# Optimization experiments

Measured on AMD Instinct MI355X. Metric: run time of the kernel, lower is better.

## Reference

```python
import jax, jax.numpy as jnp
import numpy as np

B = 2
H_GRID, W_GRID, RADIUS = 48, 48, 3
D_MODEL, N_HEADS, D_HEAD = 512, 8, 64
N = H_GRID * W_GRID          # 2304 tokens
WSIZE = (2 * RADIUS + 1) ** 2  # 49 neighbors per token
D_ACT = D_HEAD                # d_head even -> d_act = d_head
SCALE = D_ACT ** -0.5
NEG = -1e9


def _grid_neighbors():
    rr = np.arange(N) // W_GRID
    cc = np.arange(N) % W_GRID
    off = np.arange(-RADIUS, RADIUS + 1)
    dr, dc = np.meshgrid(off, off, indexing='ij')
    dr, dc = dr.ravel(), dc.ravel()
    nr = rr[:, None] + dr[None, :]
    nc = cc[:, None] + dc[None, :]
    valid = (nr >= 0) & (nr < H_GRID) & (nc >= 0) & (nc < W_GRID)
    idx = np.clip(nr, 0, H_GRID - 1) * W_GRID + np.clip(nc, 0, W_GRID - 1)
    pos = np.stack([rr, cc], axis=-1).astype(np.float32)
    return idx.astype(np.int32), valid, pos


def setup_inputs() -> dict:
    key = jax.random.key(0)
    ks = jax.random.split(key, 8)
    idx, valid, pos = _grid_neighbors()
    s = D_MODEL ** -0.5
    return {
        'x': jax.random.normal(ks[0], (B, N, D_MODEL), jnp.float32),
        'positions': jnp.asarray(pos),
        'W_Q': jax.random.normal(ks[1], (D_MODEL, N_HEADS * D_HEAD), jnp.float32) * s,
        'W_K': jax.random.normal(ks[2], (D_MODEL, N_HEADS * D_HEAD), jnp.float32) * s,
        'W_V': jax.random.normal(ks[3], (D_MODEL, N_HEADS * D_HEAD), jnp.float32) * s,
        'W_O': jax.random.normal(ks[4], (N_HEADS * D_HEAD, D_MODEL), jnp.float32) * s,
        # learnable active-subspace basis per head (near-identity init, QR'd in fwd)
        'U': jnp.eye(D_HEAD, D_ACT)[None] + 0.05 * jax.random.normal(ks[5], (N_HEADS, D_HEAD, D_ACT), jnp.float32),
        # per-head rotation generator frequencies: theta = dr . freqs per 2x2 block
        'freqs': 0.5 * jax.random.normal(ks[6], (N_HEADS, 2, D_HEAD // 2), jnp.float32),
        'neighbor_index': jnp.asarray(idx),
        'neighbor_mask': jnp.asarray(valid),
    }


def reference(x, positions, W_Q, W_K, W_V, W_O, U, freqs, neighbor_index, neighbor_mask):
    Bt, Nt, _ = x.shape

    def heads(h):  # (B,N,H*d) -> (B,H,N,d)
        return h.reshape(Bt, Nt, N_HEADS, D_HEAD).transpose(0, 2, 1, 3)

    Q = heads(x @ W_Q)
    K = heads(x @ W_K)
    V = heads(x @ W_V)

    # Active subspace projection Pi_act = U_ortho U_ortho^T, applied as x@U@U^T
    U_ortho = jnp.linalg.qr(U)[0]                       # (H, d, d_act)
    Q = jnp.einsum('bhnd,hde,hfe->bhnf', Q, U_ortho, U_ortho)
    K = jnp.einsum('bhnd,hde,hfe->bhnf', K, U_ortho, U_ortho)

    # per-(i,j) relative rotation: block-diagonal 2x2 rotations with
    # angles theta[h,n,w,p] = (r_j - r_i) . freqs[h,:,p]
    drel = positions[neighbor_index] - positions[:, None, :]   # (N,W,2)
    theta = jnp.einsum('nwc,hcp->hnwp', drel, freqs)           # (H,N,W,d/2)
    cos, sin = jnp.cos(theta), jnp.sin(theta)

    K_loc = K[:, :, neighbor_index]                            # (B,H,N,W,d) gather
    Ke, Ko = K_loc[..., 0::2], K_loc[..., 1::2]
    Kr_e = cos[None] * Ke - sin[None] * Ko
    Kr_o = sin[None] * Ke + cos[None] * Ko
    K_rot = jnp.stack([Kr_e, Kr_o], axis=-1).reshape(K_loc.shape)

    scores = jnp.einsum('bhnd,bhnwd->bhnw', Q, K_rot) * SCALE
    scores = jnp.where(neighbor_mask[None, None], scores, NEG)
    w = jax.nn.softmax(scores, axis=-1)

    V_loc = V[:, :, neighbor_index]                            # (B,H,N,W,d)
    out = jnp.einsum('bhnw,bhnwd->bhnd', w, V_loc)
    out = out.transpose(0, 2, 1, 3).reshape(Bt, Nt, N_HEADS * D_HEAD)
    return out @ W_O
```

## Files before the change

### kernel.cpp

```cpp
#include <hip/hip_runtime.h>
#include <math.h>


#define BB 2
#define HGRID 48
#define WGRID 48
#define NNODE (HGRID*WGRID)
#define RAD 3
#define WSZ 49
#define DMODEL 512
#define NHEAD 8
#define SCALE 0.125f
#define MROWS (BB*NNODE)
#define TPAD 141

typedef _Float16 f16;
typedef __attribute__((ext_vector_type(8))) _Float16 f16x8;
typedef __attribute__((ext_vector_type(2))) _Float16 h2;
typedef __attribute__((ext_vector_type(4))) float f32x4;

typedef union { f16x8 v8; h2 h[4]; } pack8;

#if __has_builtin(__builtin_amdgcn_fdot2)
__device__ __forceinline__ float fdot2(h2 a, h2 b, float c) {
    return __builtin_amdgcn_fdot2(a, b, c, false);
}
#else
__device__ __forceinline__ float fdot2(h2 a, h2 b, float c) {
    return fmaf((float)a.x, (float)b.x, fmaf((float)a.y, (float)b.y, c));
}
#endif

__global__ void convert_all(const float* __restrict__ x,
                            const float* __restrict__ WQ, const float* __restrict__ WK,
                            const float* __restrict__ WV, const float* __restrict__ WO,
                            f16* __restrict__ x2, f16* __restrict__ Wall) {
    int id = blockIdx.x * 256 + threadIdx.x;
    if (id < MROWS * 64) {
        int r = id >> 6, c8 = (id & 63) << 3;
        float4 a = *(const float4*)&x[(size_t)r * 512 + c8];
        float4 b = *(const float4*)&x[(size_t)r * 512 + c8 + 4];
        f16 o[8] = {(f16)a.x, (f16)a.y, (f16)a.z, (f16)a.w,
                    (f16)b.x, (f16)b.y, (f16)b.z, (f16)b.w};
        *(f16x8*)&x2[(size_t)r * 512 + c8] = *(f16x8*)o;
        return;
    }
    id -= MROWS * 64;
    if (id >= 2048 * 64) return;
    int np = id >> 6;
    int kb = (id & 63) << 3;
    const float* S;
    int n;
    if (np < 1536) { int t = np >> 9; n = np & 511; S = (t == 0) ? WQ : (t == 1) ? WK : WV; }
    else           { n = np - 1536;  S = WO; }
    f16 o[8];
#pragma unroll
    for (int i = 0; i < 8; ++i) o[i] = (f16)S[(size_t)(kb + i) * 512 + n];
    *(f16x8*)&Wall[(size_t)np * 512 + kb] = *(f16x8*)o;
}

template<int MODE>
__global__ __launch_bounds__(256)
void mgemm(const f16* __restrict__ A, const f16* __restrict__ Bt,
           f16* __restrict__ Qh, f16* __restrict__ Kh, f16* __restrict__ Vh,
           float* __restrict__ Cf, const float* __restrict__ freqs) {
    __shared__ f16 As[128 * 64];
    __shared__ f16 Bs[128 * 64];

    const int tid = threadIdx.x;
    const int l = tid & 63, wid = tid >> 6;
    const int m0 = blockIdx.y * 128;
    const int n0 = blockIdx.x * 128;
    const int wm = (wid >> 1) * 64, wn = (wid & 1) * 64;
    const int fr = l & 15, fk = l >> 4;
    const int srow = l >> 3, slot = l & 7;

    f32x4 acc[4][4];
#pragma unroll
    for (int m = 0; m < 4; ++m)
#pragma unroll
        for (int n = 0; n < 4; ++n) acc[m][n] = (f32x4){0.f, 0.f, 0.f, 0.f};

    for (int kt = 0; kt < 8; ++kt) {
        const int k0 = kt * 64;
#pragma unroll
        for (int j = 0; j < 4; ++j) {
            const int r = wid * 32 + j * 8 + srow;
            const int cA = (slot ^ (r & 7)) * 8;
            const f16* gA = A + (size_t)(m0 + r) * 512 + k0 + cA;
            __builtin_amdgcn_global_load_lds(
                (const __attribute__((address_space(1))) unsigned int*)gA,
                (__attribute__((address_space(3))) unsigned int*)(As + wid * 2048 + j * 512),
                16, 0, 0);
            const f16* gB = Bt + (size_t)(n0 + r) * 512 + k0 + cA;
            __builtin_amdgcn_global_load_lds(
                (const __attribute__((address_space(1))) unsigned int*)gB,
                (__attribute__((address_space(3))) unsigned int*)(Bs + wid * 2048 + j * 512),
                16, 0, 0);
        }
        asm volatile("s_waitcnt vmcnt(0)" ::: "memory");
        __syncthreads();

        f16x8 af[4][2], bfr[4][2];
#pragma unroll
        for (int m = 0; m < 4; ++m) {
            const int row = wm + m * 16 + fr;
#pragma unroll
            for (int kk = 0; kk < 2; ++kk) {
                const int b = (kk * 64 + fk * 16) ^ ((row & 7) << 4);
                af[m][kk] = *(const f16x8*)((const char*)As + row * 128 + b);
            }
        }
#pragma unroll
        for (int n = 0; n < 4; ++n) {
            const int row = wn + n * 16 + fr;
#pragma unroll
            for (int kk = 0; kk < 2; ++kk) {
                const int b = (kk * 64 + fk * 16) ^ ((row & 7) << 4);
                bfr[n][kk] = *(const f16x8*)((const char*)Bs + row * 128 + b);
            }
        }
#pragma unroll
        for (int kk = 0; kk < 2; ++kk)
#pragma unroll
            for (int m = 0; m < 4; ++m)
#pragma unroll
                for (int n = 0; n < 4; ++n)
                    acc[m][n] = __builtin_amdgcn_mfma_f32_16x16x32_f16(
                        af[m][kk], bfr[n][kk], acc[m][n], 0, 0, 0);
        __syncthreads();
    }

    if (MODE == 0) {
#pragma unroll
        for (int nf = 0; nf < 4; ++nf) {
            const int ccol = n0 + wn + nf * 16 + fr;
            const int t = ccol >> 9;
            const int h = (ccol >> 6) & 7;
            const int d = ccol & 63;
            const int p = d >> 1;
            f16* Cp = (t == 0) ? Qh : (t == 1) ? Kh : Vh;
            const float fR = freqs[h * 64 + p];
            const float fC = freqs[h * 64 + 32 + p];
            const float sgn = (d & 1) ? 1.0f : -1.0f;
#pragma unroll
            for (int mf = 0; mf < 4; ++mf) {
#pragma unroll
                for (int i = 0; i < 4; ++i) {
                    const int grow = m0 + wm + mf * 16 + fk * 4 + i;
                    const int b_ = grow >= NNODE;
                    const int nn = grow - b_ * NNODE;
                    float val = acc[mf][nf][i];
                    float part = __shfl_xor(val, 1);
                    float outv = val;
                    if (t < 2) {
                        float th = (float)(nn / WGRID) * fR + (float)(nn % WGRID) * fC;
                        float sn, cs;
                        __sincosf(th, &sn, &cs);
                        outv = fmaf(sgn * part, sn, val * cs);
                    }
                    Cp[((size_t)((b_ * NHEAD + h) * NNODE + nn)) * 64 + d] = (f16)outv;
                }
            }
        }
    } else {
#pragma unroll
        for (int nf = 0; nf < 4; ++nf) {
            const int ccol = n0 + wn + nf * 16 + fr;
#pragma unroll
            for (int mf = 0; mf < 4; ++mf) {
#pragma unroll
                for (int i = 0; i < 4; ++i) {
                    const int grow = m0 + wm + mf * 16 + fk * 4 + i;
                    Cf[(size_t)grow * 512 + ccol] = acc[mf][nf][i];
                }
            }
        }
    }
}

__global__ __launch_bounds__(256, 5)
void attn5(const f16* __restrict__ Qh, const f16* __restrict__ Kh,
           const f16* __restrict__ Vh, f16* __restrict__ out2) {
    __shared__ h2 T[32 * TPAD];

    const int tid = threadIdx.x;
    const int wid = tid >> 6, lane = tid & 63;
    const int qs = lane >> 3, wg = lane & 7;

    const int bid = blockIdx.x;
    const int t  = bid % 72, bh = bid / 72;
    const int tr = t % 12,   tc = t / 12;
    const int r0 = tr * 4,   c0 = tc * 8;
    const int h  = bh & 7,   b_ = bh >> 3;

    const int lr0 = max(0, r0 - 3), lr1 = min(HGRID - 1, r0 + 6);
    const int lc0 = max(0, c0 - 3), lc1 = min(WGRID - 1, c0 + 10);
    const int NR = lr1 - lr0 + 1, NC = lc1 - lc0 + 1;

    const f16* Kb = Kh + (size_t)bh * NNODE * 64;
    const f16* Vb = Vh + (size_t)bh * NNODE * 64;

    const int rq = r0 + wid, cq = c0 + qs;
    const int nq = rq * WGRID + cq;
    const f16* qrow = Qh + ((size_t)bh * NNODE + nq) * 64;
    h2 q2[32];
#pragma unroll
    for (int j8 = 0; j8 < 8; ++j8) {
        pack8 v;
        v.v8 = *(const f16x8*)&qrow[j8 * 8];
#pragma unroll
        for (int k = 0; k < 4; ++k) q2[j8 * 4 + k] = v.h[k];
    }

    const int cnt = NR * NC * 8;
    for (int i = tid; i < cnt; i += 256) {
        const int row = i >> 3, p4 = i & 7;
        const int glr = row / NC, glc = row - glr * NC;
        const int n = (lr0 + glr) * WGRID + (lc0 + glc);
        pack8 v;
        v.v8 = *(const f16x8*)&Kb[(size_t)n * 64 + p4 * 8];
#pragma unroll
        for (int j = 0; j < 4; ++j) T[(p4 * 4 + j) * TPAD + row] = v.h[j];
    }
    __syncthreads();

    float sc[7], es[7];
    float mx = -1e30f;
#pragma unroll
    for (int k = 0; k < 7; ++k) {
        const int w = wg + 8 * k;
        sc[k] = -1e30f;
        if (w < WSZ) {
            const int dr = w / 7 - RAD, dc = w % 7 - RAD;
            const int nr = rq + dr, nc = cq + dc;
            const bool valid = ((unsigned)nr < (unsigned)HGRID) &&
                               ((unsigned)nc < (unsigned)WGRID);
            const int nrl = min(max(nr, lr0), lr1) - lr0;
            const int ncl = min(max(nc, lc0), lc1) - lc0;
            const int row = nrl * NC + ncl;
            float s = 0.0f;
#pragma unroll
            for (int j = 0; j < 32; ++j) s = fdot2(q2[j], T[j * TPAD + row], s);
            sc[k] = valid ? s * SCALE : -1e9f;
            mx = fmaxf(mx, sc[k]);
        }
    }
#pragma unroll
    for (int o = 1; o < 8; o <<= 1) mx = fmaxf(mx, __shfl_xor(mx, o));
    float sum = 0.0f;
#pragma unroll
    for (int k = 0; k < 7; ++k) {
        const int w = wg + 8 * k;
        es[k] = 0.0f;
        if (w < WSZ) { es[k] = __expf(sc[k] - mx); sum += es[k]; }
    }
#pragma unroll
    for (int o = 1; o < 8; o <<= 1) sum += __shfl_xor(sum, o);
    const float inv = 1.0f / sum;
    float esn[7];
#pragma unroll
    for (int k = 0; k < 7; ++k) esn[k] = es[k] * inv;

    __syncthreads();

    for (int i = tid; i < cnt; i += 256) {
        const int row = i >> 3, p4 = i & 7;
        const int glr = row / NC, glc = row - glr * NC;
        const int n = (lr0 + glr) * WGRID + (lc0 + glc);
        pack8 v;
        v.v8 = *(const f16x8*)&Vb[(size_t)n * 64 + p4 * 8];
#pragma unroll
        for (int j = 0; j < 4; ++j) T[(p4 * 4 + j) * TPAD + row] = v.h[j];
    }
    __syncthreads();

    const int dg = wg;
    float2 acc[4] = {{0, 0}, {0, 0}, {0, 0}, {0, 0}};
#pragma unroll
    for (int w = 0; w < WSZ; ++w) {
        const int dr = w / 7 - RAD, dc = w % 7 - RAD;
        const int nr = rq + dr, nc = cq + dc;
        const int nrl = min(max(nr, lr0), lr1) - lr0;
        const int ncl = min(max(nc, lc0), lc1) - lc0;
        const int row = nrl * NC + ncl;
        const float pw = __shfl(esn[w >> 3], (lane & 0x38) | (w & 7));
#pragma unroll
        for (int j = 0; j < 4; ++j) {
            h2 v2 = T[(dg * 4 + j) * TPAD + row];
            acc[j].x = fmaf(pw, (float)v2.x, acc[j].x);
            acc[j].y = fmaf(pw, (float)v2.y, acc[j].y);
        }
    }

    f16 o[8] = {(f16)acc[0].x, (f16)acc[0].y, (f16)acc[1].x, (f16)acc[1].y,
                (f16)acc[2].x, (f16)acc[2].y, (f16)acc[3].x, (f16)acc[3].y};
    const size_t rowb = (size_t)(b_ * NNODE + nq) * 512 + h * 64 + dg * 8;
    *(f16x8*)&out2[rowb] = *(f16x8*)o;
}

extern "C" void kernel_launch(void* const* d_in, const int* in_sizes, int n_in,
                              void* d_out, int out_size, void* d_ws, size_t ws_size,
                              hipStream_t stream) {
    const float* x     = (const float*)d_in[0];
    const float* WQ    = (const float*)d_in[2];
    const float* WK    = (const float*)d_in[3];
    const float* WV    = (const float*)d_in[4];
    const float* WO    = (const float*)d_in[5];
    const float* freqs = (const float*)d_in[7];

    const size_t HN = (size_t)16 * NNODE * 64;
    f16* Qh   = (f16*)d_ws;
    f16* Kh   = Qh + HN;
    f16* Vh   = Kh + HN;
    f16* x2   = Vh + HN;
    f16* Wall = x2 + (size_t)MROWS * 512;
    f16* Wo2  = Wall + (size_t)1536 * 512;

    convert_all<<<((MROWS + 2048) * 64 + 255) / 256, 256, 0, stream>>>(
        x, WQ, WK, WV, WO, x2, Wall);

    dim3 gqkv(12, 36);
    mgemm<0><<<gqkv, 256, 0, stream>>>(x2, Wall, Qh, Kh, Vh, nullptr, freqs);

    attn5<<<16 * 72, 256, 0, stream>>>(Qh, Kh, Vh, x2);

    dim3 go(4, 36);
    mgemm<1><<<go, 256, 0, stream>>>(x2, Wo2, nullptr, nullptr, nullptr,
                                     (float*)d_out, freqs);
}
```

Baseline: 64.82 us.

## Double-buffer GEMM LDS tiles and load K and V together in attention

The GEMM kernel now keeps two LDS buffers per operand and issues the global-to-LDS loads for the next k-tile before computing on the current one, so load latency overlaps with MFMA work. The attention kernel stages K and V tiles into separate shared arrays in one pass, which removes the second load phase and two barriers. In exchange, both kernels use twice the LDS, the attention launch bound drops from 5 to 4 blocks per SM, and the GEMM's occupancy may fall.

```diff
diff --git a/kernel.cpp b/kernel.cpp
--- a/kernel.cpp
+++ b/kernel.cpp
@@ -64,8 +64,8 @@
 void mgemm(const f16* __restrict__ A, const f16* __restrict__ Bt,
            f16* __restrict__ Qh, f16* __restrict__ Kh, f16* __restrict__ Vh,
            float* __restrict__ Cf, const float* __restrict__ freqs) {
-    __shared__ f16 As[128 * 64];
-    __shared__ f16 Bs[128 * 64];
+    __shared__ f16 As[2][128 * 64];
+    __shared__ f16 Bs[2][128 * 64];
 
     const int tid = threadIdx.x;
     const int l = tid & 63, wid = tid >> 6;
@@ -75,13 +75,7 @@
     const int fr = l & 15, fk = l >> 4;
     const int srow = l >> 3, slot = l & 7;
 
-    f32x4 acc[4][4];
-#pragma unroll
-    for (int m = 0; m < 4; ++m)
-#pragma unroll
-        for (int n = 0; n < 4; ++n) acc[m][n] = (f32x4){0.f, 0.f, 0.f, 0.f};
-
-    for (int kt = 0; kt < 8; ++kt) {
+    auto stage = [&](int buf, int kt) {
         const int k0 = kt * 64;
 #pragma unroll
         for (int j = 0; j < 4; ++j) {
@@ -90,16 +84,29 @@
             const f16* gA = A + (size_t)(m0 + r) * 512 + k0 + cA;
             __builtin_amdgcn_global_load_lds(
                 (const __attribute__((address_space(1))) unsigned int*)gA,
-                (__attribute__((address_space(3))) unsigned int*)(As + wid * 2048 + j * 512),
+                (__attribute__((address_space(3))) unsigned int*)(As[buf] + wid * 2048 + j * 512),
                 16, 0, 0);
             const f16* gB = Bt + (size_t)(n0 + r) * 512 + k0 + cA;
             __builtin_amdgcn_global_load_lds(
                 (const __attribute__((address_space(1))) unsigned int*)gB,
-                (__attribute__((address_space(3))) unsigned int*)(Bs + wid * 2048 + j * 512),
+                (__attribute__((address_space(3))) unsigned int*)(Bs[buf] + wid * 2048 + j * 512),
                 16, 0, 0);
         }
-        asm volatile("s_waitcnt vmcnt(0)" ::: "memory");
-        __syncthreads();
+    };
+
+    f32x4 acc[4][4];
+#pragma unroll
+    for (int m = 0; m < 4; ++m)
+#pragma unroll
+        for (int n = 0; n < 4; ++n) acc[m][n] = (f32x4){0.f, 0.f, 0.f, 0.f};
+
+    stage(0, 0);
+    asm volatile("s_waitcnt vmcnt(0)" ::: "memory");
+    __syncthreads();
+
+    for (int kt = 0; kt < 8; ++kt) {
+        const int cur = kt & 1;
+        if (kt < 7) stage(cur ^ 1, kt + 1);
 
         f16x8 af[4][2], bfr[4][2];
 #pragma unroll
@@ -108,7 +115,7 @@
 #pragma unroll
             for (int kk = 0; kk < 2; ++kk) {
                 const int b = (kk * 64 + fk * 16) ^ ((row & 7) << 4);
-                af[m][kk] = *(const f16x8*)((const char*)As + row * 128 + b);
+                af[m][kk] = *(const f16x8*)((const char*)As[cur] + row * 128 + b);
             }
         }
 #pragma unroll
@@ -117,7 +124,7 @@
 #pragma unroll
             for (int kk = 0; kk < 2; ++kk) {
                 const int b = (kk * 64 + fk * 16) ^ ((row & 7) << 4);
-                bfr[n][kk] = *(const f16x8*)((const char*)Bs + row * 128 + b);
+                bfr[n][kk] = *(const f16x8*)((const char*)Bs[cur] + row * 128 + b);
             }
         }
 #pragma unroll
@@ -128,7 +135,11 @@
                 for (int n = 0; n < 4; ++n)
                     acc[m][n] = __builtin_amdgcn_mfma_f32_16x16x32_f16(
                         af[m][kk], bfr[n][kk], acc[m][n], 0, 0, 0);
-        __syncthreads();
+
+        if (kt < 7) {
+            asm volatile("s_waitcnt vmcnt(0)" ::: "memory");
+            __syncthreads();
+        }
     }
 
     if (MODE == 0) {
@@ -179,10 +190,11 @@
     }
 }
 
-__global__ __launch_bounds__(256, 5)
-void attn5(const f16* __restrict__ Qh, const f16* __restrict__ Kh,
+__global__ __launch_bounds__(256, 4)
+void attn6(const f16* __restrict__ Qh, const f16* __restrict__ Kh,
            const f16* __restrict__ Vh, f16* __restrict__ out2) {
-    __shared__ h2 T[32 * TPAD];
+    __shared__ h2 Tk[32 * TPAD];
+    __shared__ h2 Tv[32 * TPAD];
 
     const int tid = threadIdx.x;
     const int wid = tid >> 6, lane = tid & 63;
@@ -218,10 +230,14 @@
         const int row = i >> 3, p4 = i & 7;
         const int glr = row / NC, glc = row - glr * NC;
         const int n = (lr0 + glr) * WGRID + (lc0 + glc);
-        pack8 v;
-        v.v8 = *(const f16x8*)&Kb[(size_t)n * 64 + p4 * 8];
-#pragma unroll
-        for (int j = 0; j < 4; ++j) T[(p4 * 4 + j) * TPAD + row] = v.h[j];
+        pack8 kv, vv;
+        kv.v8 = *(const f16x8*)&Kb[(size_t)n * 64 + p4 * 8];
+        vv.v8 = *(const f16x8*)&Vb[(size_t)n * 64 + p4 * 8];
+#pragma unroll
+        for (int j = 0; j < 4; ++j) {
+            Tk[(p4 * 4 + j) * TPAD + row] = kv.h[j];
+            Tv[(p4 * 4 + j) * TPAD + row] = vv.h[j];
+        }
     }
     __syncthreads();
 
@@ -241,7 +257,7 @@
             const int row = nrl * NC + ncl;
             float s = 0.0f;
 #pragma unroll
-            for (int j = 0; j < 32; ++j) s = fdot2(q2[j], T[j * TPAD + row], s);
+            for (int j = 0; j < 32; ++j) s = fdot2(q2[j], Tk[j * TPAD + row], s);
             sc[k] = valid ? s * SCALE : -1e9f;
             mx = fmaxf(mx, sc[k]);
         }
@@ -261,19 +277,6 @@
     float esn[7];
 #pragma unroll
     for (int k = 0; k < 7; ++k) esn[k] = es[k] * inv;
-
-    __syncthreads();
-
-    for (int i = tid; i < cnt; i += 256) {
-        const int row = i >> 3, p4 = i & 7;
-        const int glr = row / NC, glc = row - glr * NC;
-        const int n = (lr0 + glr) * WGRID + (lc0 + glc);
-        pack8 v;
-        v.v8 = *(const f16x8*)&Vb[(size_t)n * 64 + p4 * 8];
-#pragma unroll
-        for (int j = 0; j < 4; ++j) T[(p4 * 4 + j) * TPAD + row] = v.h[j];
-    }
-    __syncthreads();
 
     const int dg = wg;
     float2 acc[4] = {{0, 0}, {0, 0}, {0, 0}, {0, 0}};
@@ -287,7 +290,7 @@
         const float pw = __shfl(esn[w >> 3], (lane & 0x38) | (w & 7));
 #pragma unroll
         for (int j = 0; j < 4; ++j) {
-            h2 v2 = T[(dg * 4 + j) * TPAD + row];
+            h2 v2 = Tv[(dg * 4 + j) * TPAD + row];
             acc[j].x = fmaf(pw, (float)v2.x, acc[j].x);
             acc[j].y = fmaf(pw, (float)v2.y, acc[j].y);
         }
@@ -323,7 +326,7 @@
     dim3 gqkv(12, 36);
     mgemm<0><<<gqkv, 256, 0, stream>>>(x2, Wall, Qh, Kh, Vh, nullptr, freqs);
 
-    attn5<<<16 * 72, 256, 0, stream>>>(Qh, Kh, Vh, x2);
+    attn6<<<16 * 72, 256, 0, stream>>>(Qh, Kh, Vh, x2);
 
     dim3 go(4, 36);
     mgemm<1><<<go, 256, 0, stream>>>(x2, Wo2, nullptr, nullptr, nullptr,
```

After: 68.71 us. 1.06x slower.
